# Optimization experiments

Measured on AMD Instinct MI355X. Metric: run time of the kernel, lower is better.

## Reference

```python
import jax, jax.numpy as jnp
import numpy as np

D_MODEL = 1024
N_HEADS = 16
D_K = D_MODEL // N_HEADS


def _glorot(key, fan_in, fan_out):
    limit = np.sqrt(6.0 / (fan_in + fan_out)).astype(np.float32)
    return jax.random.uniform(key, (fan_in, fan_out), jnp.float32, -limit, limit)


def setup_inputs() -> dict:
    key = jax.random.key(0)
    kx, kq, kk, kv = jax.random.split(key, 4)
    x = jax.random.normal(kx, (2, 2048, D_MODEL), jnp.float32)
    Wq = _glorot(kq, D_MODEL, D_MODEL)
    Wk = _glorot(kk, D_MODEL, D_MODEL)
    Wv = _glorot(kv, D_MODEL, D_MODEL)
    bq = jnp.zeros((D_MODEL,), jnp.float32)
    bk = jnp.zeros((D_MODEL,), jnp.float32)
    bv = jnp.zeros((D_MODEL,), jnp.float32)
    return {"x": x, "Wq": Wq, "bq": bq, "Wk": Wk, "bk": bk, "Wv": Wv, "bv": bv}


def reference(x, Wq, bq, Wk, bk, Wv, bv):
    B, S, _ = x.shape
    # QKV projections (Dense layers with bias)
    q = (x @ Wq + bq).reshape(B, S, N_HEADS, D_K).transpose(0, 2, 1, 3)  # [B,H,S,Dk]
    k = (x @ Wk + bk).reshape(B, S, N_HEADS, D_K).transpose(0, 2, 1, 3)
    v = (x @ Wv + bv).reshape(B, S, N_HEADS, D_K).transpose(0, 2, 1, 3)
    # raw exp-based softmax (NO max subtraction, per original module)
    scores = jnp.einsum('bhqd,bhkd->bhqk', q, k) / np.sqrt(D_K).astype(np.float32)
    scores = jnp.exp(scores)
    attn = scores / (jnp.sum(scores, axis=-1, keepdims=True) + 1e-8)
    context = jnp.einsum('bhqk,bhkd->bhqd', attn, v)  # [B,H,S,Dk]
    return context.transpose(0, 2, 1, 3).reshape(B, S, N_HEADS * D_K)
```

## Files before the change

### kernel.cpp

```cpp
#include <hip/hip_runtime.h>
#include <hip/hip_bf16.h>
#include <stdint.h>

typedef __bf16 bf16x8 __attribute__((ext_vector_type(8)));
typedef __bf16 bf16x4 __attribute__((ext_vector_type(4)));
typedef float  f32x4  __attribute__((ext_vector_type(4)));
typedef short  s16x4  __attribute__((ext_vector_type(4)));
typedef short  s16x8  __attribute__((ext_vector_type(8)));
typedef unsigned short u16_t;

#define MFMA(a, b, c)   __builtin_amdgcn_mfma_f32_16x16x32_bf16((a), (b), (c), 0, 0, 0)

__device__ __forceinline__ bf16x8 cat8(s16x4 a, s16x4 b) {
  s16x8 t = __builtin_shufflevector(a, b, 0, 1, 2, 3, 4, 5, 6, 7);
  return *(bf16x8*)&t;
}
__device__ __forceinline__ bf16x8 b8(s16x8 v) {
  bf16x8 r; __builtin_memcpy(&r, &v, 16); return r;
}

__device__ __forceinline__ void cp16(const void* g, void* l) {
  __builtin_amdgcn_global_load_lds(
      (const __attribute__((address_space(1))) unsigned int*)g,
      (__attribute__((address_space(3))) unsigned int*)l, 16, 0, 0);
}

__global__ __launch_bounds__(256) void k_prep(const float* __restrict__ x,
                                              const float* __restrict__ W0,
                                              const float* __restrict__ W1,
                                              const float* __restrict__ W2,
                                              u16_t* __restrict__ xb,
                                              u16_t* __restrict__ Wt) {
  __shared__ u16_t T[64][65];
  int bx = blockIdx.x, t = threadIdx.x;
  if (bx < 4096) {
    int i = bx * 256 + t;
    float4 f = ((const float4*)x)[i];
    bf16x4 o = {(__bf16)f.x, (__bf16)f.y, (__bf16)f.z, (__bf16)f.w};
    *(bf16x4*)&xb[(size_t)i * 4] = o;
    return;
  }
  int j = bx - 4096;
  int nx = j & 15, ny = (j >> 4) & 15, z = j >> 8;
  const float* W = z == 0 ? W0 : (z == 1 ? W1 : W2);
  int k0 = ny * 64, n0 = nx * 64;
#pragma unroll
  for (int i = 0; i < 16; i++) {
    int e = i * 256 + t, r = e >> 6, c = e & 63;
    __bf16 hv = (__bf16)W[(size_t)(k0 + r) * 1024 + n0 + c];
    T[r][c] = *(u16_t*)&hv;
  }
  __syncthreads();
  size_t base = ((size_t)z * 1024 + n0) * 1024 + k0;
#pragma unroll
  for (int i = 0; i < 16; i++) {
    int e = i * 256 + t, r = e >> 6, c = e & 63;
    Wt[base + (size_t)r * 1024 + c] = T[c][r];
  }
}

__global__ __launch_bounds__(512, 2) void k_gemm_qkv(
    const u16_t* __restrict__ A, const u16_t* __restrict__ Bt,
    const float* __restrict__ bq, const float* __restrict__ bk,
    const float* __restrict__ bv,
    u16_t* __restrict__ Qo, u16_t* __restrict__ Ko, u16_t* __restrict__ Vo) {
  __shared__ u16_t smem[57344];
  u16_t* As = smem;
  u16_t* Bs = smem + 32768;

  const int tid = threadIdx.x, lane = tid & 63, wv = tid >> 6;
  const int quad = lane >> 4, col = lane & 15;
  const int wm = wv >> 2, wn = wv & 3;

  int bid = blockIdx.x;
  int wg = (bid & 7) * 32 + (bid >> 3);
  const int tn = (wg & 15) * 192, tm = (wg >> 4) << 8;

  const int r16 = lane >> 2, c4 = lane & 3;
  const int srow = wv * 16 + r16;
  const int skoff = ((c4 ^ ((r16 >> 1) & 3)) << 3);
  const int sdst = srow * 32 + (c4 << 3);
  const size_t gA0 = (size_t)(tm + srow) * 1024 + skoff;
  const size_t gB0 = (size_t)(tn + srow) * 1024 + skoff;

  f32x4 acc[8][3] = {};

#define STAGE(kt, h, b) do {                                     \
    int dA_ = (b) * 16384 + (h) * 8192 + sdst;                   \
    int dB_ = (b) * 12288 + (h) * 6144 + sdst;                   \
    size_t s_ = (size_t)(kt) * 64 + (h) * 32;                    \
    cp16(A + gA0 + s_, As + dA_);                                \
    cp16(A + gA0 + s_ + (size_t)128 * 1024, As + dA_ + 4096);    \
    cp16(Bt + gB0 + s_, Bs + dB_);                               \
    if (wv < 4)                                                  \
      cp16(Bt + gB0 + s_ + (size_t)128 * 1024, Bs + dB_ + 4096); \
  } while (0)

#define BAR()    asm volatile("s_barrier" ::: "memory")
#define WAITV(N) asm volatile("s_waitcnt vmcnt(" #N ")" ::: "memory")
#define WAITL()  asm volatile("s_waitcnt lgkmcnt(0)" ::: "memory")
#define SCHED0() __builtin_amdgcn_sched_barrier(0)

  STAGE(0, 0, 0);
  STAGE(0, 1, 0);
  WAITV(3);
  BAR();

  const int swz8 = (((lane >> 4) ^ ((col >> 1) & 3)) << 3);
  const int abase = (wm * 128 + col) * 32 + swz8;
  const int bbase = (wn * 48 + col) * 32 + swz8;

  for (int t = 0; t < 16; ++t) {
    const int cur = t & 1, nxt = cur ^ 1;
    const u16_t* Ap = As + cur * 16384;
    const u16_t* Bp = Bs + cur * 12288;
    bf16x8 af[4], bf[3];

#pragma unroll
    for (int i = 0; i < 4; i++) af[i] = *(const bf16x8*)&Ap[abase + i * 512];
#pragma unroll
    for (int j = 0; j < 3; j++) bf[j] = *(const bf16x8*)&Bp[bbase + j * 512];
    if (t + 1 < 16) STAGE(t + 1, 0, nxt);
    BAR(); WAITL(); SCHED0();
    __builtin_amdgcn_s_setprio(1);
#pragma unroll
    for (int i = 0; i < 4; i++)
#pragma unroll
      for (int j = 0; j < 3; j++) acc[i][j] = MFMA(af[i], bf[j], acc[i][j]);
    __builtin_amdgcn_s_setprio(0);
    BAR();

#pragma unroll
    for (int i = 0; i < 4; i++) af[i] = *(const bf16x8*)&Ap[abase + (i + 4) * 512];
    if (t + 1 < 16) { STAGE(t + 1, 1, nxt); WAITV(6); }
    else            { WAITV(0); }
    BAR(); WAITL(); SCHED0();
    __builtin_amdgcn_s_setprio(1);
#pragma unroll
    for (int i = 0; i < 4; i++)
#pragma unroll
      for (int j = 0; j < 3; j++) acc[i + 4][j] = MFMA(af[i], bf[j], acc[i + 4][j]);
    __builtin_amdgcn_s_setprio(0);
    BAR();

#pragma unroll
    for (int i = 0; i < 4; i++) af[i] = *(const bf16x8*)&Ap[8192 + abase + i * 512];
#pragma unroll
    for (int j = 0; j < 3; j++) bf[j] = *(const bf16x8*)&Bp[6144 + bbase + j * 512];
    BAR(); WAITL(); SCHED0();
    __builtin_amdgcn_s_setprio(1);
#pragma unroll
    for (int i = 0; i < 4; i++)
#pragma unroll
      for (int j = 0; j < 3; j++) acc[i][j] = MFMA(af[i], bf[j], acc[i][j]);
    __builtin_amdgcn_s_setprio(0);
    BAR();

#pragma unroll
    for (int i = 0; i < 4; i++) af[i] = *(const bf16x8*)&Ap[8192 + abase + (i + 4) * 512];
    if (t + 1 < 16) WAITV(3);
    WAITL();
    BAR(); SCHED0();
    __builtin_amdgcn_s_setprio(1);
#pragma unroll
    for (int i = 0; i < 4; i++)
#pragma unroll
      for (int j = 0; j < 3; j++) acc[i + 4][j] = MFMA(af[i], bf[j], acc[i + 4][j]);
    __builtin_amdgcn_s_setprio(0);
    BAR();
  }

#undef STAGE

#pragma unroll
  for (int nt = 0; nt < 3; nt++) {
    int gn = tn + wn * 48 + nt * 16 + col;
    int mat = gn >> 10, d = gn & 1023, h = d >> 6, dk = d & 63;
    const float* bias = mat == 0 ? bq : (mat == 1 ? bk : bv);
    float bb = bias[d];
    if (mat == 2) {
#pragma unroll
      for (int mt = 0; mt < 8; mt++) {
        int gm = tm + wm * 128 + mt * 16 + quad * 4;
        int b = gm >> 11, s = gm & 2047;
        bf16x4 pk4;
#pragma unroll
        for (int r = 0; r < 4; r++) pk4[r] = (__bf16)(acc[mt][nt][r] + bb);
        *(bf16x4*)&Vo[((size_t)((b * 16 + h) * 64 + dk)) * 2048 + s] = pk4;
      }
    } else {
      u16_t* O = mat == 0 ? Qo : Ko;
      const float scl = mat == 0 ? 0.18033688011112042f : 1.0f;
#pragma unroll
      for (int mt = 0; mt < 8; mt++) {
#pragma unroll
        for (int r = 0; r < 4; r++) {
          int gm = tm + wm * 128 + mt * 16 + quad * 4 + r;
          int b = gm >> 11, s = gm & 2047;
          __bf16 hv = (__bf16)((acc[mt][nt][r] + bb) * scl);
          O[((size_t)((b * 16 + h) * 2048 + s)) * 64 + dk] = *(u16_t*)&hv;
        }
      }
    }
  }
}

__global__ __launch_bounds__(256, 4) void k_attn(const u16_t* __restrict__ Q,
                                                 const u16_t* __restrict__ K,
                                                 const u16_t* __restrict__ Vt,
                                                 float* __restrict__ out) {
  __shared__ u16_t smem[20480];
  u16_t* Qs  = smem;
  u16_t* Ksb = smem + 4096;
  u16_t* Vsb = smem + 12288;
  const int tid = threadIdx.x, lane = tid & 63, wv = tid >> 6;
  const int quad = lane >> 4, col = lane & 15;
  const int qh = wv >> 1, kh = wv & 1;

  const int bid = blockIdx.x;
  const int bh = (bid & 7) + 8 * ((bid >> 3) >> 5);
  const int qt = (bid >> 3) & 31;
  const int b = bh >> 4, h = bh & 15;
  const int r8 = lane >> 3, c8 = lane & 7;

  const u16_t* Qg = Q + ((size_t)bh * 2048 + qt * 64) * 64;
  const u16_t* Kg = K + (size_t)bh * 2048 * 64;
  const u16_t* Vg = Vt + (size_t)bh * 64 * 2048;

  const int lch  = c8 ^ r8;
  const int row0 = (wv * 2) * 8 + r8, row1 = (wv * 2 + 1) * 8 + r8;
  const int ldst0 = (wv * 2) * 512 + lane * 8;
  const int ldst1 = (wv * 2 + 1) * 512 + lane * 8;
  const int gk0 = row0 * 64 + lch * 8,   gk1 = row1 * 64 + lch * 8;
  const int gv0 = row0 * 2048 + lch * 8, gv1 = row1 * 2048 + lch * 8;

  cp16(Qg + gk0, Qs + ldst0);
  cp16(Qg + gk1, Qs + ldst1);
  cp16(Kg + gk0, Ksb + ldst0);
  cp16(Kg + gk1, Ksb + ldst1);
  __syncthreads();

  bf16x8 qf[2][2];
#pragma unroll
  for (int nt = 0; nt < 2; nt++)
#pragma unroll
    for (int ks = 0; ks < 2; ks++) {
      int row = qh * 32 + nt * 16 + col;
      qf[nt][ks] = *(const bf16x8*)&Qs[row * 64 + (((ks * 4 + quad) ^ (row & 7)) * 8)];
    }

  int ka[2][2];
#pragma unroll
  for (int ks = 0; ks < 2; ks++)
#pragma unroll
    for (int mt = 0; mt < 2; mt++) {
      int row = kh * 32 + mt * 16 + col;
      ka[ks][mt] = row * 64 + (((ks * 4 + quad) ^ (row & 7)) * 8);
    }
  int va0[4], va1[4];
#pragma unroll
  for (int dt = 0; dt < 4; dt++) {
    int row = dt * 16 + col;
    int cc = kh * 4 + (quad >> 1);
    va0[dt] = row * 64 + ((cc ^ (row & 7)) * 8) + (quad & 1) * 4;
    va1[dt] = row * 64 + (((cc + 2) ^ (row & 7)) * 8) + (quad & 1) * 4;
  }

  const short one_bf = (short)0x3F80;
  s16x8 ones8s = {one_bf, one_bf, one_bf, one_bf, one_bf, one_bf, one_bf, one_bf};
  const bf16x8 ones8 = *(bf16x8*)&ones8s;
  const f32x4 z4 = {0.f, 0.f, 0.f, 0.f};

  f32x4 ao[2][4] = {};
  f32x4 dn[2] = {};
  s16x8 pA[2] = {}, pB[2] = {};

#define ATTN_STEP(KT, CUR, PFW, PFR, DO_PV, DO_PRE) do {                              \
    const u16_t* Kc = Ksb + (CUR) * 4096;                                             \
    const u16_t* Vp = Vsb + ((CUR) ^ 1) * 4096;                                       \
    u16_t* Kn = Ksb + ((CUR) ^ 1) * 4096;                                             \
    u16_t* Vn = Vsb + (CUR) * 4096;                                                   \
    if (DO_PRE) {                                                                     \
      const u16_t* kb = Kg + (size_t)((KT) + 1) * 4096;                               \
      cp16(kb + gk0, Kn + ldst0);                                                     \
      cp16(kb + gk1, Kn + ldst1);                                                     \
    }                                                                                 \
    {                                                                                 \
      const u16_t* vb = Vg + (size_t)(KT) * 64;                                       \
      cp16(vb + gv0, Vn + ldst0);                                                     \
      cp16(vb + gv1, Vn + ldst1);                                                     \
    }                                                                                 \
    f32x4 sc[2][2];                                                                   \
    __builtin_amdgcn_s_setprio(1);                                                    \
    {                                                                                 \
      bf16x8 kf0 = *(const bf16x8*)&Kc[ka[0][0]];                                     \
      bf16x8 kf1 = *(const bf16x8*)&Kc[ka[0][1]];                                     \
      sc[0][0] = MFMA(kf0, qf[0][0], z4);                                             \
      sc[0][1] = MFMA(kf0, qf[1][0], z4);                                             \
      sc[1][0] = MFMA(kf1, qf[0][0], z4);                                             \
      sc[1][1] = MFMA(kf1, qf[1][0], z4);                                             \
      kf0 = *(const bf16x8*)&Kc[ka[1][0]];                                            \
      kf1 = *(const bf16x8*)&Kc[ka[1][1]];                                            \
      sc[0][0] = MFMA(kf0, qf[0][1], sc[0][0]);                                       \
      sc[0][1] = MFMA(kf0, qf[1][1], sc[0][1]);                                       \
      sc[1][0] = MFMA(kf1, qf[0][1], sc[1][0]);                                       \
      sc[1][1] = MFMA(kf1, qf[1][1], sc[1][1]);                                       \
    }                                                                                 \
    if (DO_PV) {                                                                      \
      bf16x8 pa0 = b8(PFR[0]);                                                        \
      bf16x8 pa1 = b8(PFR[1]);                                                        \
      _Pragma("unroll")                                                               \
      for (int dt = 0; dt < 4; dt++) {                                                \
        bf16x8 vv = cat8(*(const s16x4*)&Vp[va0[dt]], *(const s16x4*)&Vp[va1[dt]]);   \
        ao[0][dt] = MFMA(pa0, vv, ao[0][dt]);                                         \
        ao[1][dt] = MFMA(pa1, vv, ao[1][dt]);                                         \
      }                                                                               \
    }                                                                                 \
    __builtin_amdgcn_s_setprio(0);                                                    \
    _Pragma("unroll")                                                                 \
    for (int mt = 0; mt < 2; mt++)                                                    \
      _Pragma("unroll")                                                               \
      for (int nt = 0; nt < 2; nt++)                                                  \
        _Pragma("unroll")                                                             \
        for (int r = 0; r < 4; r++) {                                                 \
          __bf16 e = (__bf16)__builtin_amdgcn_exp2f(sc[mt][nt][r]);                   \
          PFW[nt][mt * 4 + r] = *(short*)&e;                                          \
        }                                                                             \
    dn[0] = MFMA(b8(PFW[0]), ones8, dn[0]);                                           \
    dn[1] = MFMA(b8(PFW[1]), ones8, dn[1]);                                           \
    __syncthreads();                                                                  \
  } while (0)

  ATTN_STEP(0, 0, pA, pB, 0, 1);
  ATTN_STEP(1, 1, pB, pA, 1, 1);
#pragma unroll 1
  for (int kt2 = 1; kt2 < 15; kt2++) {
    int kt0 = kt2 * 2;
    ATTN_STEP(kt0,     0, pA, pB, 1, 1);
    ATTN_STEP(kt0 + 1, 1, pB, pA, 1, 1);
  }
  ATTN_STEP(30, 0, pA, pB, 1, 1);
  ATTN_STEP(31, 1, pB, pA, 1, 0);
#undef ATTN_STEP

  {
    const u16_t* Vp = Vsb + 4096;
    bf16x8 pa0 = b8(pB[0]);
    bf16x8 pa1 = b8(pB[1]);
#pragma unroll
    for (int dt = 0; dt < 4; dt++) {
      bf16x8 vv = cat8(*(const s16x4*)&Vp[va0[dt]], *(const s16x4*)&Vp[va1[dt]]);
      ao[0][dt] = MFMA(pa0, vv, ao[0][dt]);
      ao[1][dt] = MFMA(pa1, vv, ao[1][dt]);
    }
  }

  float* red = (float*)(smem + 4096);
  const int rb = (qh * 64 + lane) * 41;
  if (kh == 1) {
#pragma unroll
    for (int nt = 0; nt < 2; nt++) {
#pragma unroll
      for (int dt = 0; dt < 4; dt++)
#pragma unroll
        for (int r = 0; r < 4; r++)
          red[rb + (nt * 4 + dt) * 4 + r] = ao[nt][dt][r];
#pragma unroll
      for (int r = 0; r < 4; r++)
        red[rb + 32 + nt * 4 + r] = dn[nt][r];
    }
  }
  __syncthreads();
  if (kh == 0) {
#pragma unroll
    for (int nt = 0; nt < 2; nt++) {
      float inv[4];
#pragma unroll
      for (int r = 0; r < 4; r++)
        inv[r] = 1.0f / (dn[nt][r] + red[rb + 32 + nt * 4 + r] + 1e-8f);
#pragma unroll
      for (int dt = 0; dt < 4; dt++) {
#pragma unroll
        for (int r = 0; r < 4; r++) {
          float v = (ao[nt][dt][r] + red[rb + (nt * 4 + dt) * 4 + r]) * inv[r];
          int s = qt * 64 + qh * 32 + nt * 16 + quad * 4 + r;
          out[((size_t)b * 2048 + s) * 1024 + h * 64 + dt * 16 + col] = v;
        }
      }
    }
  }
}

extern "C" void kernel_launch(void* const* d_in, const int* in_sizes, int n_in,
                              void* d_out, int out_size, void* d_ws, size_t ws_size,
                              hipStream_t stream) {
  const float* x  = (const float*)d_in[0];
  const float* Wq = (const float*)d_in[1];
  const float* bq = (const float*)d_in[2];
  const float* Wk = (const float*)d_in[3];
  const float* bk = (const float*)d_in[4];
  const float* Wv = (const float*)d_in[5];
  const float* bv = (const float*)d_in[6];
  float* out = (float*)d_out;

  char* ws = (char*)d_ws;
  u16_t* xb  = (u16_t*)(ws);
  u16_t* Wt  = (u16_t*)(ws + 8388608);
  u16_t* Qb  = (u16_t*)(ws + 14680064);
  u16_t* Kb  = (u16_t*)(ws + 23068672);
  u16_t* Vtb = (u16_t*)(ws + 31457280);

  hipLaunchKernelGGL(k_prep, dim3(4864), dim3(256), 0, stream, x, Wq, Wk, Wv, xb, Wt);
  hipLaunchKernelGGL(k_gemm_qkv, dim3(256), dim3(512), 0, stream,
                     xb, Wt, bq, bk, bv, Qb, Kb, Vtb);
  hipLaunchKernelGGL(k_attn, dim3(1024), dim3(256), 0, stream, Qb, Kb, Vtb, out);
}
```

Baseline: 167.8 us.

## Enlarge attention query tile to 128 rows and drop key-split reduction

The attention kernel now gives each block 128 query rows, 32 per wave, instead of 64 rows, and each wave covers the full 64-key tile rather than half of it. This doubles reuse of every K/V tile loaded into shared memory, halves the grid, and removes the cross-wave shared-memory reduction and its extra barrier at the end. In exchange, per-wave registers and shared memory grow, launch bounds drop to 2 blocks per SM, and the grid of 512 blocks may fill the compute units less evenly.

Result: faster. 159.9 us (-4.7%).

```diff
diff --git a/kernel.cpp b/kernel.cpp
--- a/kernel.cpp
+++ b/kernel.cpp
@@ -205,25 +205,24 @@
   }
 }
 
-__global__ __launch_bounds__(256, 4) void k_attn(const u16_t* __restrict__ Q,
+__global__ __launch_bounds__(256, 2) void k_attn(const u16_t* __restrict__ Q,
                                                  const u16_t* __restrict__ K,
                                                  const u16_t* __restrict__ Vt,
                                                  float* __restrict__ out) {
-  __shared__ u16_t smem[20480];
+  __shared__ u16_t smem[24576];
   u16_t* Qs  = smem;
-  u16_t* Ksb = smem + 4096;
-  u16_t* Vsb = smem + 12288;
+  u16_t* Ksb = smem + 8192;
+  u16_t* Vsb = smem + 16384;
   const int tid = threadIdx.x, lane = tid & 63, wv = tid >> 6;
   const int quad = lane >> 4, col = lane & 15;
-  const int qh = wv >> 1, kh = wv & 1;
 
   const int bid = blockIdx.x;
-  const int bh = (bid & 7) + 8 * ((bid >> 3) >> 5);
-  const int qt = (bid >> 3) & 31;
+  const int bh = (bid & 7) + 8 * ((bid >> 3) >> 4);
+  const int qt = (bid >> 3) & 15;
   const int b = bh >> 4, h = bh & 15;
   const int r8 = lane >> 3, c8 = lane & 7;
 
-  const u16_t* Qg = Q + ((size_t)bh * 2048 + qt * 64) * 64;
+  const u16_t* Qg = Q + ((size_t)bh * 2048 + qt * 128) * 64;
   const u16_t* Kg = K + (size_t)bh * 2048 * 64;
   const u16_t* Vg = Vt + (size_t)bh * 64 * 2048;
 
@@ -234,8 +233,11 @@
   const int gk0 = row0 * 64 + lch * 8,   gk1 = row1 * 64 + lch * 8;
   const int gv0 = row0 * 2048 + lch * 8, gv1 = row1 * 2048 + lch * 8;
 
-  cp16(Qg + gk0, Qs + ldst0);
-  cp16(Qg + gk1, Qs + ldst1);
+#pragma unroll
+  for (int i = 0; i < 4; i++) {
+    int c = wv * 4 + i;
+    cp16(Qg + (c * 8 + r8) * 64 + lch * 8, Qs + c * 512 + lane * 8);
+  }
   cp16(Kg + gk0, Ksb + ldst0);
   cp16(Kg + gk1, Ksb + ldst1);
   __syncthreads();
@@ -245,26 +247,28 @@
   for (int nt = 0; nt < 2; nt++)
 #pragma unroll
     for (int ks = 0; ks < 2; ks++) {
-      int row = qh * 32 + nt * 16 + col;
+      int row = wv * 32 + nt * 16 + col;
       qf[nt][ks] = *(const bf16x8*)&Qs[row * 64 + (((ks * 4 + quad) ^ (row & 7)) * 8)];
     }
 
-  int ka[2][2];
+  int ka[2][4];
 #pragma unroll
   for (int ks = 0; ks < 2; ks++)
 #pragma unroll
-    for (int mt = 0; mt < 2; mt++) {
-      int row = kh * 32 + mt * 16 + col;
+    for (int mt = 0; mt < 4; mt++) {
+      int row = mt * 16 + col;
       ka[ks][mt] = row * 64 + (((ks * 4 + quad) ^ (row & 7)) * 8);
     }
-  int va0[4], va1[4];
-#pragma unroll
-  for (int dt = 0; dt < 4; dt++) {
-    int row = dt * 16 + col;
-    int cc = kh * 4 + (quad >> 1);
-    va0[dt] = row * 64 + ((cc ^ (row & 7)) * 8) + (quad & 1) * 4;
-    va1[dt] = row * 64 + (((cc + 2) ^ (row & 7)) * 8) + (quad & 1) * 4;
-  }
+  int va0[2][4], va1[2][4];
+#pragma unroll
+  for (int g = 0; g < 2; g++)
+#pragma unroll
+    for (int dt = 0; dt < 4; dt++) {
+      int row = dt * 16 + col;
+      int cc = g * 4 + (quad >> 1);
+      va0[g][dt] = row * 64 + ((cc ^ (row & 7)) * 8) + (quad & 1) * 4;
+      va1[g][dt] = row * 64 + (((cc + 2) ^ (row & 7)) * 8) + (quad & 1) * 4;
+    }
 
   const short one_bf = (short)0x3F80;
   s16x8 ones8s = {one_bf, one_bf, one_bf, one_bf, one_bf, one_bf, one_bf, one_bf};
@@ -273,7 +277,7 @@
 
   f32x4 ao[2][4] = {};
   f32x4 dn[2] = {};
-  s16x8 pA[2] = {}, pB[2] = {};
+  s16x8 pA[2][2] = {}, pB[2][2] = {};
 
 #define ATTN_STEP(KT, CUR, PFW, PFR, DO_PV, DO_PRE) do {                              \
     const u16_t* Kc = Ksb + (CUR) * 4096;                                             \
@@ -290,44 +294,49 @@
       cp16(vb + gv0, Vn + ldst0);                                                     \
       cp16(vb + gv1, Vn + ldst1);                                                     \
     }                                                                                 \
-    f32x4 sc[2][2];                                                                   \
+    f32x4 sc[4][2];                                                                   \
     __builtin_amdgcn_s_setprio(1);                                                    \
-    {                                                                                 \
-      bf16x8 kf0 = *(const bf16x8*)&Kc[ka[0][0]];                                     \
-      bf16x8 kf1 = *(const bf16x8*)&Kc[ka[0][1]];                                     \
-      sc[0][0] = MFMA(kf0, qf[0][0], z4);                                             \
-      sc[0][1] = MFMA(kf0, qf[1][0], z4);                                             \
-      sc[1][0] = MFMA(kf1, qf[0][0], z4);                                             \
-      sc[1][1] = MFMA(kf1, qf[1][0], z4);                                             \
-      kf0 = *(const bf16x8*)&Kc[ka[1][0]];                                            \
-      kf1 = *(const bf16x8*)&Kc[ka[1][1]];                                            \
-      sc[0][0] = MFMA(kf0, qf[0][1], sc[0][0]);                                       \
-      sc[0][1] = MFMA(kf0, qf[1][1], sc[0][1]);                                       \
-      sc[1][0] = MFMA(kf1, qf[0][1], sc[1][0]);                                       \
-      sc[1][1] = MFMA(kf1, qf[1][1], sc[1][1]);                                       \
+    _Pragma("unroll")                                                                 \
+    for (int ks = 0; ks < 2; ks++) {                                                  \
+      bf16x8 kf[4];                                                                   \
+      _Pragma("unroll")                                                               \
+      for (int mt = 0; mt < 4; mt++) kf[mt] = *(const bf16x8*)&Kc[ka[ks][mt]];        \
+      _Pragma("unroll")                                                               \
+      for (int mt = 0; mt < 4; mt++)                                                  \
+        _Pragma("unroll")                                                             \
+        for (int nt = 0; nt < 2; nt++)                                                \
+          sc[mt][nt] = ks ? MFMA(kf[mt], qf[nt][1], sc[mt][nt])                       \
+                          : MFMA(kf[mt], qf[nt][0], z4);                              \
     }                                                                                 \
     if (DO_PV) {                                                                      \
-      bf16x8 pa0 = b8(PFR[0]);                                                        \
-      bf16x8 pa1 = b8(PFR[1]);                                                        \
+      bf16x8 pa00 = b8(PFR[0][0]), pa01 = b8(PFR[0][1]);                              \
+      bf16x8 pa10 = b8(PFR[1][0]), pa11 = b8(PFR[1][1]);                              \
       _Pragma("unroll")                                                               \
       for (int dt = 0; dt < 4; dt++) {                                                \
-        bf16x8 vv = cat8(*(const s16x4*)&Vp[va0[dt]], *(const s16x4*)&Vp[va1[dt]]);   \
-        ao[0][dt] = MFMA(pa0, vv, ao[0][dt]);                                         \
-        ao[1][dt] = MFMA(pa1, vv, ao[1][dt]);                                         \
+        bf16x8 vv0 = cat8(*(const s16x4*)&Vp[va0[0][dt]],                             \
+                          *(const s16x4*)&Vp[va1[0][dt]]);                            \
+        bf16x8 vv1 = cat8(*(const s16x4*)&Vp[va0[1][dt]],                             \
+                          *(const s16x4*)&Vp[va1[1][dt]]);                            \
+        ao[0][dt] = MFMA(pa00, vv0, ao[0][dt]);                                       \
+        ao[0][dt] = MFMA(pa01, vv1, ao[0][dt]);                                       \
+        ao[1][dt] = MFMA(pa10, vv0, ao[1][dt]);                                       \
+        ao[1][dt] = MFMA(pa11, vv1, ao[1][dt]);                                       \
       }                                                                               \
     }                                                                                 \
     __builtin_amdgcn_s_setprio(0);                                                    \
     _Pragma("unroll")                                                                 \
-    for (int mt = 0; mt < 2; mt++)                                                    \
+    for (int mt = 0; mt < 4; mt++)                                                    \
       _Pragma("unroll")                                                               \
       for (int nt = 0; nt < 2; nt++)                                                  \
         _Pragma("unroll")                                                             \
         for (int r = 0; r < 4; r++) {                                                 \
           __bf16 e = (__bf16)__builtin_amdgcn_exp2f(sc[mt][nt][r]);                   \
-          PFW[nt][mt * 4 + r] = *(short*)&e;                                          \
+          PFW[nt][mt >> 1][(mt & 1) * 4 + r] = *(short*)&e;                           \
         }                                                                             \
-    dn[0] = MFMA(b8(PFW[0]), ones8, dn[0]);                                           \
-    dn[1] = MFMA(b8(PFW[1]), ones8, dn[1]);                                           \
+    dn[0] = MFMA(b8(PFW[0][0]), ones8, dn[0]);                                        \
+    dn[0] = MFMA(b8(PFW[0][1]), ones8, dn[0]);                                        \
+    dn[1] = MFMA(b8(PFW[1][0]), ones8, dn[1]);                                        \
+    dn[1] = MFMA(b8(PFW[1][1]), ones8, dn[1]);                                        \
     __syncthreads();                                                                  \
   } while (0)
 
@@ -345,47 +354,32 @@
 
   {
     const u16_t* Vp = Vsb + 4096;
-    bf16x8 pa0 = b8(pB[0]);
-    bf16x8 pa1 = b8(pB[1]);
+    bf16x8 pa00 = b8(pB[0][0]), pa01 = b8(pB[0][1]);
+    bf16x8 pa10 = b8(pB[1][0]), pa11 = b8(pB[1][1]);
 #pragma unroll
     for (int dt = 0; dt < 4; dt++) {
-      bf16x8 vv = cat8(*(const s16x4*)&Vp[va0[dt]], *(const s16x4*)&Vp[va1[dt]]);
-      ao[0][dt] = MFMA(pa0, vv, ao[0][dt]);
-      ao[1][dt] = MFMA(pa1, vv, ao[1][dt]);
-    }
-  }
-
-  float* red = (float*)(smem + 4096);
-  const int rb = (qh * 64 + lane) * 41;
-  if (kh == 1) {
-#pragma unroll
-    for (int nt = 0; nt < 2; nt++) {
-#pragma unroll
-      for (int dt = 0; dt < 4; dt++)
-#pragma unroll
-        for (int r = 0; r < 4; r++)
-          red[rb + (nt * 4 + dt) * 4 + r] = ao[nt][dt][r];
-#pragma unroll
-      for (int r = 0; r < 4; r++)
-        red[rb + 32 + nt * 4 + r] = dn[nt][r];
-    }
-  }
-  __syncthreads();
-  if (kh == 0) {
-#pragma unroll
-    for (int nt = 0; nt < 2; nt++) {
-      float inv[4];
-#pragma unroll
-      for (int r = 0; r < 4; r++)
-        inv[r] = 1.0f / (dn[nt][r] + red[rb + 32 + nt * 4 + r] + 1e-8f);
-#pragma unroll
-      for (int dt = 0; dt < 4; dt++) {
-#pragma unroll
-        for (int r = 0; r < 4; r++) {
-          float v = (ao[nt][dt][r] + red[rb + (nt * 4 + dt) * 4 + r]) * inv[r];
-          int s = qt * 64 + qh * 32 + nt * 16 + quad * 4 + r;
-          out[((size_t)b * 2048 + s) * 1024 + h * 64 + dt * 16 + col] = v;
-        }
+      bf16x8 vv0 = cat8(*(const s16x4*)&Vp[va0[0][dt]], *(const s16x4*)&Vp[va1[0][dt]]);
+      bf16x8 vv1 = cat8(*(const s16x4*)&Vp[va0[1][dt]], *(const s16x4*)&Vp[va1[1][dt]]);
+      ao[0][dt] = MFMA(pa00, vv0, ao[0][dt]);
+      ao[0][dt] = MFMA(pa01, vv1, ao[0][dt]);
+      ao[1][dt] = MFMA(pa10, vv0, ao[1][dt]);
+      ao[1][dt] = MFMA(pa11, vv1, ao[1][dt]);
+    }
+  }
+
+#pragma unroll
+  for (int nt = 0; nt < 2; nt++) {
+    float inv[4];
+#pragma unroll
+    for (int r = 0; r < 4; r++)
+      inv[r] = 1.0f / (dn[nt][r] + 1e-8f);
+#pragma unroll
+    for (int dt = 0; dt < 4; dt++) {
+#pragma unroll
+      for (int r = 0; r < 4; r++) {
+        float v = ao[nt][dt][r] * inv[r];
+        int s = qt * 128 + wv * 32 + nt * 16 + quad * 4 + r;
+        out[((size_t)b * 2048 + s) * 1024 + h * 64 + dt * 16 + col] = v;
       }
     }
   }
@@ -413,5 +407,5 @@
   hipLaunchKernelGGL(k_prep, dim3(4864), dim3(256), 0, stream, x, Wq, Wk, Wv, xb, Wt);
   hipLaunchKernelGGL(k_gemm_qkv, dim3(256), dim3(512), 0, stream,
                      xb, Wt, bq, bk, bv, Qb, Kb, Vtb);
-  hipLaunchKernelGGL(k_attn, dim3(1024), dim3(256), 0, stream, Qb, Kb, Vtb, out);
-}
+  hipLaunchKernelGGL(k_attn, dim3(512), dim3(256), 0, stream, Qb, Kb, Vtb, out);
+}
```
